# Performance work log

Hardware: AMD Instinct MI355X
Metric: run time of the kernel (lower is better)

Reference implementation:

```python
import jax, jax.numpy as jnp
import numpy as np

D_MODEL = 1024
NUM_HEADS = 16
D_K = D_MODEL // NUM_HEADS
ROPE_THETA = 10000.0


def setup_inputs() -> dict:
    key = jax.random.key(0)
    kx, kq, kk, kv, ko = jax.random.split(key, 5)
    B, S = 4, 2048
    std = (2.0 / (D_MODEL + D_MODEL)) ** 0.5
    def w(k):
        return jax.random.truncated_normal(k, -3.0, 3.0, (D_MODEL, D_MODEL), jnp.float32) * std
    return {
        "x": jax.random.normal(kx, (B, S, D_MODEL), jnp.float32),
        "Wq": w(kq), "Wk": w(kk), "Wv": w(kv), "Wo": w(ko),
    }


def _apply_rope(t):
    # t: [B, H, S, d_k]
    S, dk = t.shape[-2], t.shape[-1]
    inv_freq = 1.0 / (ROPE_THETA ** (jnp.arange(0, dk, 2) / dk))  # [dk/2]
    angles = jnp.outer(jnp.arange(S), inv_freq)                    # [S, dk/2]
    cos = jnp.repeat(jnp.cos(angles), 2, axis=-1).astype(t.dtype)  # [S, dk]
    sin = jnp.repeat(jnp.sin(angles), 2, axis=-1).astype(t.dtype)
    t_even = t[..., 0::2]
    t_odd = t[..., 1::2]
    t_rot = jnp.stack([-t_odd, t_even], axis=-1).reshape(t.shape)
    return t * cos + t_rot * sin


def reference(x, Wq, Wk, Wv, Wo):
    B, S, D = x.shape
    H, dk = NUM_HEADS, D_K
    q = jnp.einsum("bsi,io->bso", x, Wq).reshape(B, S, H, dk).swapaxes(1, 2)
    k = jnp.einsum("bsi,io->bso", x, Wk).reshape(B, S, H, dk).swapaxes(1, 2)
    v = jnp.einsum("bsi,io->bso", x, Wv).reshape(B, S, H, dk).swapaxes(1, 2)
    q = _apply_rope(q)
    k = _apply_rope(k)
    scores = jnp.einsum("bhqd,bhkd->bhqk", q, k) / (dk ** 0.5)  # [B,H,S,S]
    causal = jnp.tril(jnp.ones((S, S), dtype=bool))
    scores = jnp.where(causal, scores, -jnp.inf)
    attn = jax.nn.softmax(scores, axis=-1)
    out = jnp.einsum("bhqk,bhkd->bhqd", attn, v)  # [B,H,S,dk]
    out = out.swapaxes(1, 2).reshape(B, S, D)
    return jnp.einsum("bsi,io->bso", out, Wo)
```

## Files before the change

kernel.cpp:

```cpp
#include <hip/hip_runtime.h>
#include <hip/hip_bf16.h>

#define SEQ   2048
#define NB    4
#define NH    16
#define DK    64
#define DM    1024
#define MROWS (NB * SEQ)

typedef __bf16 bf16_t;
typedef __bf16 bf16x8 __attribute__((ext_vector_type(8)));
typedef __bf16 bf16x4 __attribute__((ext_vector_type(4)));
typedef float  f32x4  __attribute__((ext_vector_type(4)));

#define MFMA16(a, b, c) __builtin_amdgcn_mfma_f32_16x16x32_bf16((a), (b), (c), 0, 0, 0)

__device__ __forceinline__ void gl2lds16(const bf16_t* g, bf16_t* l) {
    __builtin_amdgcn_global_load_lds(
        (const __attribute__((address_space(1))) unsigned int*)g,
        (__attribute__((address_space(3))) unsigned int*)l, 16, 0, 0);
}

__global__ __launch_bounds__(256) void cvt_kernel(
    const float* __restrict__ in, bf16_t* __restrict__ out, int n)
{
    int i = (blockIdx.x * 256 + threadIdx.x) * 4;
    if (i + 3 < n) {
        const float4 v = *(const float4*)(in + i);
        bf16x4 o;
        o[0] = (bf16_t)v.x; o[1] = (bf16_t)v.y;
        o[2] = (bf16_t)v.z; o[3] = (bf16_t)v.w;
        *(bf16x4*)(out + i) = o;
    }
}

__global__ __launch_bounds__(256) void wtr_kernel(
    const float* __restrict__ W, bf16_t* __restrict__ Wt)
{
    __shared__ float T[32][33];
    const int tk0 = (blockIdx.x >> 5) << 5;
    const int tn0 = (blockIdx.x & 31) << 5;
    const int r = threadIdx.x >> 5, c = threadIdx.x & 31;
#pragma unroll
    for (int i = 0; i < 4; ++i)
        T[r + i * 8][c] = W[(size_t)(tk0 + r + i * 8) * DM + tn0 + c];
    __syncthreads();
#pragma unroll
    for (int i = 0; i < 4; ++i)
        Wt[(size_t)(tn0 + r + i * 8) * DM + tk0 + c] = (bf16_t)T[c][r + i * 8];
}

__global__ void rope_table_kernel(float2* __restrict__ tab) {
    int idx = blockIdx.x * 256 + threadIdx.x;
    if (idx >= SEQ * 32) return;
    int s = idx >> 5, i = idx & 31;
    float freq = powf(10000.0f, -(float)i / 32.0f);
    float a = (float)s * freq;
    tab[idx] = make_float2(cosf(a), sinf(a));
}

template<bool TR>
__device__ __forceinline__ void kloop128(
    const bf16_t* __restrict__ Xp, const bf16_t* __restrict__ Wp,
    bf16_t* As, bf16_t* Bs, int tid, f32x4 (&acc)[4][4], int kiters)
{
    const int lane = tid & 63;
    const int wave = tid >> 6;
    const int wm = wave & 1, wn = wave >> 1;
    const int l = lane & 15, quad = lane >> 4;
    const int rl = lane & 15;
    const int kf = (lane >> 4) << 3;
    const int gA = wave * 2;

    const bf16_t* xa0 = Xp + (size_t)(gA * 16 + rl) * DM + kf;
    const bf16_t* xa1 = Xp + (size_t)((gA + 1) * 16 + rl) * DM + kf;
    const bf16_t* wb0 = Wp + (size_t)(gA * 16 + rl) * DM + kf;
    const bf16_t* wb1 = Wp + (size_t)((gA + 1) * 16 + rl) * DM + kf;

    gl2lds16(xa0, As + gA * 512);
    gl2lds16(xa1, As + (gA + 1) * 512);
    gl2lds16(wb0, Bs + gA * 512);
    gl2lds16(wb1, Bs + (gA + 1) * 512);

    for (int k = 0; k < kiters; ++k) {
        const int cur = k & 1;
        __syncthreads();
        if (k + 1 < kiters) {
            const int nxt = cur ^ 1;
            const int ko = (k + 1) * 32;
            gl2lds16(xa0 + ko, As + nxt * 4096 + gA * 512);
            gl2lds16(xa1 + ko, As + nxt * 4096 + (gA + 1) * 512);
            gl2lds16(wb0 + ko, Bs + nxt * 4096 + gA * 512);
            gl2lds16(wb1 + ko, Bs + nxt * 4096 + (gA + 1) * 512);
        }
        const bf16_t* ab = As + cur * 4096;
        const bf16_t* bb = Bs + cur * 4096;
        bf16x8 af[4], bw[4];
#pragma unroll
        for (int a = 0; a < 4; ++a) {
            af[a] = *(const bf16x8*)(ab + (wm * 4 + a) * 512 + (quad * 16 + l) * 8);
            bw[a] = *(const bf16x8*)(bb + (wn * 4 + a) * 512 + (quad * 16 + l) * 8);
        }
#pragma unroll
        for (int a = 0; a < 4; ++a)
#pragma unroll
            for (int b = 0; b < 4; ++b)
                acc[a][b] = TR ? MFMA16(bw[b], af[a], acc[a][b])
                               : MFMA16(af[a], bw[b], acc[a][b]);
    }
}

__global__ __launch_bounds__(256) void gemm_qkv_kernel(
    const bf16_t* __restrict__ X, const bf16_t* __restrict__ Wt,
    bf16_t* __restrict__ Qt, bf16_t* __restrict__ Kt, bf16_t* __restrict__ Vtr,
    const float2* __restrict__ rope)
{
    __shared__ __align__(16) bf16_t As[2 * 128 * 32];
    __shared__ __align__(16) bf16_t Bs[2 * 128 * 32];

    const int tid  = threadIdx.x;
    const int lane = tid & 63;
    const int wave = tid >> 6;
    const int wm   = wave & 1, wn = wave >> 1;
    const int l    = lane & 15;
    const int quad = lane >> 4;

    const int m0 = (blockIdx.x / 24) << 7;
    const int n0 = (blockIdx.x % 24) << 7;
    const bool tr = (n0 >= 2 * DM);

    f32x4 acc[4][4] = {};
    if (tr) kloop128<true >(X + (size_t)m0 * DM, Wt + (size_t)n0 * DM, As, Bs, tid, acc, DM / 32);
    else    kloop128<false>(X + (size_t)m0 * DM, Wt + (size_t)n0 * DM, As, Bs, tid, acc, DM / 32);

#pragma unroll
    for (int a = 0; a < 4; ++a)
#pragma unroll
        for (int b = 0; b < 4; ++b)
#pragma unroll
            for (int r = 0; r < 4; ++r) {
                float v = acc[a][b][r];
                if (tr) {
                    const int n = n0 + wn * 64 + b * 16 + quad * 4 + r;
                    const int m = m0 + wm * 64 + a * 16 + l;
                    const int bi = m >> 11, s = m & (SEQ - 1);
                    const int col = n & (DM - 1);
                    const int h = col >> 6, d = col & (DK - 1);
                    Vtr[(((size_t)(bi * NH + h)) * DK + d) * SEQ + s] = (bf16_t)v;
                } else {
                    const int m  = m0 + wm * 64 + a * 16 + quad * 4 + r;
                    const int nn = n0 + wn * 64 + b * 16 + l;
                    const int bi = m >> 11, s = m & (SEQ - 1);
                    const int col = nn & (DM - 1);
                    const int h = col >> 6, d = col & (DK - 1);
                    float pv = __shfl_xor(v, 1);
                    float2 cs = rope[s * 32 + (d >> 1)];
                    float res = (d & 1) ? (v * cs.x + pv * cs.y)
                                        : (v * cs.x - pv * cs.y);
                    bf16_t* dst = (nn < DM) ? Qt : Kt;
                    if (nn < DM) res *= 0.125f;
                    dst[(((size_t)(bi * NH + h)) * SEQ + s) * DK + d] = (bf16_t)res;
                }
            }
}

__global__ __launch_bounds__(256) void gemm_out_kernel(
    const bf16_t* __restrict__ X, const bf16_t* __restrict__ Wt,
    float* __restrict__ out)
{
    __shared__ __align__(16) bf16_t As[2 * 128 * 32];
    __shared__ __align__(16) bf16_t Bs[2 * 128 * 32];

    const int tid  = threadIdx.x;
    const int lane = tid & 63;
    const int wave = tid >> 6;
    const int wm   = wave & 1, wn = wave >> 1;
    const int l    = lane & 15;
    const int quad = lane >> 4;

    const int m0 = (blockIdx.x >> 3) << 7;
    const int n0 = (blockIdx.x & 7) << 7;

    f32x4 acc[4][4] = {};
    kloop128<false>(X + (size_t)m0 * DM, Wt + (size_t)n0 * DM, As, Bs, tid, acc, DM / 32);

#pragma unroll
    for (int a = 0; a < 4; ++a)
#pragma unroll
        for (int b = 0; b < 4; ++b)
#pragma unroll
            for (int r = 0; r < 4; ++r) {
                const int m  = m0 + wm * 64 + a * 16 + quad * 4 + r;
                const int nn = n0 + wn * 64 + b * 16 + l;
                out[(size_t)m * DM + nn] = acc[a][b][r];
            }
}

#define KLD 72

__global__ __launch_bounds__(256) void attn_kernel(
    const bf16_t* __restrict__ Q, const bf16_t* __restrict__ K,
    const bf16_t* __restrict__ Vt, bf16_t* __restrict__ O)
{
    __shared__ __align__(16) bf16_t Kl[64 * KLD];
    __shared__ __align__(16) bf16_t Vl[64 * KLD];
    __shared__ __align__(16) bf16_t Pl[4][32 * KLD];

    const int bh   = blockIdx.y;
    const int tid  = threadIdx.x;
    const int wave = tid >> 6;
    const int lane = tid & 63;
    const int l    = lane & 15;
    const int quad = lane >> 4;
    const int srow = tid >> 3;
    const int sch  = (tid & 7) << 3;

    bf16_t* Pw = Pl[wave];
    const bf16_t* Qb = Q  + (size_t)bh * SEQ * DK;
    const bf16_t* Kb = K  + (size_t)bh * SEQ * DK;
    const bf16_t* Vb = Vt + (size_t)bh * DK * SEQ;
    const int b = bh >> 4, h = bh & 15;

    for (int ph = 0; ph < 2; ++ph) {
        const int qblk = ph ? (15 - (int)blockIdx.x) : (int)blockIdx.x;
        const int q0w  = qblk * 128 + wave * 32;
        const int nch  = 2 * (qblk + 1);

        bf16x8 qb[2][2];
#pragma unroll
        for (int u = 0; u < 2; ++u) {
            qb[u][0] = *(const bf16x8*)(Qb + (size_t)(q0w + u * 16 + l) * DK + quad * 8);
            qb[u][1] = *(const bf16x8*)(Qb + (size_t)(q0w + u * 16 + l) * DK + 32 + quad * 8);
        }

        float m_run[2] = {-3e38f, -3e38f};
        float l_run[2] = {0.f, 0.f};
        f32x4 o[4][2] = {};

        bf16x8 pk0 = *(const bf16x8*)(Kb + (size_t)srow * DK + sch);
        bf16x8 pk1 = *(const bf16x8*)(Kb + (size_t)(32 + srow) * DK + sch);
        bf16x8 pv0 = *(const bf16x8*)(Vb + (size_t)srow * SEQ + sch);
        bf16x8 pv1 = *(const bf16x8*)(Vb + (size_t)(32 + srow) * SEQ + sch);

        for (int i = 0; i < nch; ++i) {
            const int c = i * 64;
            __syncthreads();
            *(bf16x8*)(Kl + srow * KLD + sch)        = pk0;
            *(bf16x8*)(Kl + (32 + srow) * KLD + sch) = pk1;
            *(bf16x8*)(Vl + srow * KLD + sch)        = pv0;
            *(bf16x8*)(Vl + (32 + srow) * KLD + sch) = pv1;
            __syncthreads();
            if (i + 1 < nch) {
                const int cn = c + 64;
                pk0 = *(const bf16x8*)(Kb + (size_t)(cn + srow) * DK + sch);
                pk1 = *(const bf16x8*)(Kb + (size_t)(cn + 32 + srow) * DK + sch);
                pv0 = *(const bf16x8*)(Vb + (size_t)srow * SEQ + cn + sch);
                pv1 = *(const bf16x8*)(Vb + (size_t)(32 + srow) * SEQ + cn + sch);
            }
            if (c > q0w + 31) continue;

            f32x4 st[4][2] = {};
#pragma unroll
            for (int t = 0; t < 4; ++t) {
                const bf16x8 k0 = *(const bf16x8*)(Kl + (t * 16 + l) * KLD + quad * 8);
                const bf16x8 k1 = *(const bf16x8*)(Kl + (t * 16 + l) * KLD + 32 + quad * 8);
                st[t][0] = MFMA16(k0, qb[0][0], st[t][0]);
                st[t][0] = MFMA16(k1, qb[0][1], st[t][0]);
                st[t][1] = MFMA16(k0, qb[1][0], st[t][1]);
                st[t][1] = MFMA16(k1, qb[1][1], st[t][1]);
            }
            if (c + 63 > q0w) {
#pragma unroll
                for (int u = 0; u < 2; ++u) {
                    const int thr = q0w + u * 16 + l - c - quad * 4;
#pragma unroll
                    for (int t = 0; t < 4; ++t)
#pragma unroll
                        for (int r = 0; r < 4; ++r)
                            if (t * 16 + r > thr) st[t][u][r] = -3e38f;
                }
            }
#pragma unroll
            for (int u = 0; u < 2; ++u) {
                float cmax = -3e38f;
#pragma unroll
                for (int t = 0; t < 4; ++t)
#pragma unroll
                    for (int r = 0; r < 4; ++r)
                        cmax = fmaxf(cmax, st[t][u][r]);
                cmax = fmaxf(cmax, __shfl_xor(cmax, 16));
                cmax = fmaxf(cmax, __shfl_xor(cmax, 32));
                const float mnew  = fmaxf(m_run[u], cmax);
                const float alpha = __expf(m_run[u] - mnew);
                m_run[u] = mnew;
                float csum = 0.f;
#pragma unroll
                for (int t = 0; t < 4; ++t)
#pragma unroll
                    for (int r = 0; r < 4; ++r) {
                        st[t][u][r] = __expf(st[t][u][r] - mnew);
                        csum += st[t][u][r];
                    }
                csum += __shfl_xor(csum, 16);
                csum += __shfl_xor(csum, 32);
                l_run[u] = l_run[u] * alpha + csum;
#pragma unroll
                for (int n = 0; n < 4; ++n)
#pragma unroll
                    for (int r = 0; r < 4; ++r)
                        o[n][u][r] *= alpha;
#pragma unroll
                for (int t = 0; t < 4; ++t) {
                    bf16x4 pk;
                    pk[0] = (bf16_t)st[t][u][0]; pk[1] = (bf16_t)st[t][u][1];
                    pk[2] = (bf16_t)st[t][u][2]; pk[3] = (bf16_t)st[t][u][3];
                    *(bf16x4*)(Pw + (u * 16 + l) * KLD + t * 16 + quad * 4) = pk;
                }
            }
            const bf16x8 pb00 = *(const bf16x8*)(Pw + l * KLD + quad * 8);
            const bf16x8 pb01 = *(const bf16x8*)(Pw + l * KLD + 32 + quad * 8);
            const bf16x8 pb10 = *(const bf16x8*)(Pw + (16 + l) * KLD + quad * 8);
            const bf16x8 pb11 = *(const bf16x8*)(Pw + (16 + l) * KLD + 32 + quad * 8);
#pragma unroll
            for (int n = 0; n < 4; ++n) {
                const bf16x8 v0 = *(const bf16x8*)(Vl + (n * 16 + l) * KLD + quad * 8);
                const bf16x8 v1 = *(const bf16x8*)(Vl + (n * 16 + l) * KLD + 32 + quad * 8);
                o[n][0] = MFMA16(v0, pb00, o[n][0]);
                o[n][0] = MFMA16(v1, pb01, o[n][0]);
                o[n][1] = MFMA16(v0, pb10, o[n][1]);
                o[n][1] = MFMA16(v1, pb11, o[n][1]);
            }
        }

#pragma unroll
        for (int u = 0; u < 2; ++u) {
            const float inv = 1.0f / l_run[u];
#pragma unroll
            for (int n = 0; n < 4; ++n) {
                bf16x4 ov;
                ov[0] = (bf16_t)(o[n][u][0] * inv); ov[1] = (bf16_t)(o[n][u][1] * inv);
                ov[2] = (bf16_t)(o[n][u][2] * inv); ov[3] = (bf16_t)(o[n][u][3] * inv);
                *(bf16x4*)(Pw + (u * 16 + l) * KLD + n * 16 + quad * 4) = ov;
            }
        }
        const int row  = lane >> 1;
        const int half = (lane & 1) * 32;
        const bf16x8 w0 = *(const bf16x8*)(Pw + row * KLD + half);
        const bf16x8 w1 = *(const bf16x8*)(Pw + row * KLD + half + 8);
        const bf16x8 w2 = *(const bf16x8*)(Pw + row * KLD + half + 16);
        const bf16x8 w3 = *(const bf16x8*)(Pw + row * KLD + half + 24);
        bf16_t* op = O + ((size_t)(b * SEQ + qblk * 128 + wave * 32 + row)) * DM
                       + h * DK + half;
        *(bf16x8*)(op)      = w0;
        *(bf16x8*)(op + 8)  = w1;
        *(bf16x8*)(op + 16) = w2;
        *(bf16x8*)(op + 24) = w3;
    }
}

extern "C" void kernel_launch(void* const* d_in, const int* in_sizes, int n_in,
                              void* d_out, int out_size, void* d_ws, size_t ws_size,
                              hipStream_t stream)
{
    const float* x  = (const float*)d_in[0];
    const float* Wq = (const float*)d_in[1];
    const float* Wk = (const float*)d_in[2];
    const float* Wv = (const float*)d_in[3];
    const float* Wo = (const float*)d_in[4];

    char* ws = (char*)d_ws;
    float2* rope = (float2*)ws;
    const size_t TEN = (size_t)MROWS * DM;
    const size_t WEL = (size_t)DM * DM;
    bf16_t* xb    = (bf16_t*)(ws + (1 << 19));
    bf16_t* Wqkvt = xb + TEN;
    bf16_t* Wot   = Wqkvt + 3 * WEL;
    bf16_t* Qt    = Wot + WEL;
    bf16_t* Kt    = Qt + TEN;
    bf16_t* Vt    = Kt + TEN;
    bf16_t* Ot    = Vt + TEN;

    rope_table_kernel<<<(SEQ * 32 + 255) / 256, 256, 0, stream>>>(rope);

    cvt_kernel<<<(int)(TEN / 4 / 256), 256, 0, stream>>>(x, xb, (int)TEN);
    wtr_kernel<<<1024, 256, 0, stream>>>(Wq, Wqkvt);
    wtr_kernel<<<1024, 256, 0, stream>>>(Wk, Wqkvt + WEL);
    wtr_kernel<<<1024, 256, 0, stream>>>(Wv, Wqkvt + 2 * WEL);
    wtr_kernel<<<1024, 256, 0, stream>>>(Wo, Wot);

    gemm_qkv_kernel<<<64 * 24, 256, 0, stream>>>(xb, Wqkvt, Qt, Kt, Vt, rope);

    attn_kernel<<<dim3(8, NB * NH), 256, 0, stream>>>(Qt, Kt, Vt, Ot);

    gemm_out_kernel<<<64 * 8, 256, 0, stream>>>(Ot, Wot, (float*)d_out);
}
```

Baseline: 338.3 us.

## Shrink GEMM tiles to 128x64, reorder blocks M-fastest, merge weight transposes

Changes the QKV and output projection GEMMs from 128x128 to 128x64 output tiles. This doubles the grid size and, with launch_bounds of 4, is meant to raise occupancy, since the output GEMM previously launched only 512 blocks. Block indexing now iterates M fastest, so consecutive blocks share the same weight tile in L2. The four weight-transpose launches are merged into one 2D-grid kernel. The trade-off is lower arithmetic intensity per block and more total A-tile traffic.

```diff
diff --git a/kernel.cpp b/kernel.cpp
--- a/kernel.cpp
+++ b/kernel.cpp
@@ -34,10 +34,15 @@
     }
 }
 
-__global__ __launch_bounds__(256) void wtr_kernel(
-    const float* __restrict__ W, bf16_t* __restrict__ Wt)
+__global__ __launch_bounds__(256) void wtr4_kernel(
+    const float* __restrict__ W0, const float* __restrict__ W1,
+    const float* __restrict__ W2, const float* __restrict__ W3,
+    bf16_t* __restrict__ Wt)
 {
     __shared__ float T[32][33];
+    const int y = blockIdx.y;
+    const float* W = (y == 0) ? W0 : (y == 1) ? W1 : (y == 2) ? W2 : W3;
+    bf16_t* out = Wt + (size_t)y * DM * DM;
     const int tk0 = (blockIdx.x >> 5) << 5;
     const int tn0 = (blockIdx.x & 31) << 5;
     const int r = threadIdx.x >> 5, c = threadIdx.x & 31;
@@ -47,7 +52,7 @@
     __syncthreads();
 #pragma unroll
     for (int i = 0; i < 4; ++i)
-        Wt[(size_t)(tn0 + r + i * 8) * DM + tk0 + c] = (bf16_t)T[c][r + i * 8];
+        out[(size_t)(tn0 + r + i * 8) * DM + tk0 + c] = (bf16_t)T[c][r + i * 8];
 }
 
 __global__ void rope_table_kernel(float2* __restrict__ tab) {
@@ -60,9 +65,9 @@
 }
 
 template<bool TR>
-__device__ __forceinline__ void kloop128(
+__device__ __forceinline__ void kloop_128x64(
     const bf16_t* __restrict__ Xp, const bf16_t* __restrict__ Wp,
-    bf16_t* As, bf16_t* Bs, int tid, f32x4 (&acc)[4][4], int kiters)
+    bf16_t* As, bf16_t* Bs, int tid, f32x4 (&acc)[4][2])
 {
     const int lane = tid & 63;
     const int wave = tid >> 6;
@@ -70,53 +75,51 @@
     const int l = lane & 15, quad = lane >> 4;
     const int rl = lane & 15;
     const int kf = (lane >> 4) << 3;
-    const int gA = wave * 2;
-
-    const bf16_t* xa0 = Xp + (size_t)(gA * 16 + rl) * DM + kf;
-    const bf16_t* xa1 = Xp + (size_t)((gA + 1) * 16 + rl) * DM + kf;
-    const bf16_t* wb0 = Wp + (size_t)(gA * 16 + rl) * DM + kf;
-    const bf16_t* wb1 = Wp + (size_t)((gA + 1) * 16 + rl) * DM + kf;
-
-    gl2lds16(xa0, As + gA * 512);
-    gl2lds16(xa1, As + (gA + 1) * 512);
-    gl2lds16(wb0, Bs + gA * 512);
-    gl2lds16(wb1, Bs + (gA + 1) * 512);
-
+
+    const bf16_t* xa0 = Xp + (size_t)((wave * 2)     * 16 + rl) * DM + kf;
+    const bf16_t* xa1 = Xp + (size_t)((wave * 2 + 1) * 16 + rl) * DM + kf;
+    const bf16_t* wb0 = Wp + (size_t)(wave * 16 + rl) * DM + kf;
+
+    gl2lds16(xa0, As + (wave * 2) * 512);
+    gl2lds16(xa1, As + (wave * 2 + 1) * 512);
+    gl2lds16(wb0, Bs + wave * 512);
+
+    const int kiters = DM / 32;
     for (int k = 0; k < kiters; ++k) {
         const int cur = k & 1;
         __syncthreads();
         if (k + 1 < kiters) {
             const int nxt = cur ^ 1;
             const int ko = (k + 1) * 32;
-            gl2lds16(xa0 + ko, As + nxt * 4096 + gA * 512);
-            gl2lds16(xa1 + ko, As + nxt * 4096 + (gA + 1) * 512);
-            gl2lds16(wb0 + ko, Bs + nxt * 4096 + gA * 512);
-            gl2lds16(wb1 + ko, Bs + nxt * 4096 + (gA + 1) * 512);
+            gl2lds16(xa0 + ko, As + nxt * 4096 + (wave * 2) * 512);
+            gl2lds16(xa1 + ko, As + nxt * 4096 + (wave * 2 + 1) * 512);
+            gl2lds16(wb0 + ko, Bs + nxt * 2048 + wave * 512);
         }
         const bf16_t* ab = As + cur * 4096;
-        const bf16_t* bb = Bs + cur * 4096;
-        bf16x8 af[4], bw[4];
-#pragma unroll
-        for (int a = 0; a < 4; ++a) {
+        const bf16_t* bb = Bs + cur * 2048;
+        bf16x8 af[4], bw[2];
+#pragma unroll
+        for (int a = 0; a < 4; ++a)
             af[a] = *(const bf16x8*)(ab + (wm * 4 + a) * 512 + (quad * 16 + l) * 8);
-            bw[a] = *(const bf16x8*)(bb + (wn * 4 + a) * 512 + (quad * 16 + l) * 8);
-        }
+#pragma unroll
+        for (int b = 0; b < 2; ++b)
+            bw[b] = *(const bf16x8*)(bb + (wn * 2 + b) * 512 + (quad * 16 + l) * 8);
 #pragma unroll
         for (int a = 0; a < 4; ++a)
 #pragma unroll
-            for (int b = 0; b < 4; ++b)
+            for (int b = 0; b < 2; ++b)
                 acc[a][b] = TR ? MFMA16(bw[b], af[a], acc[a][b])
                                : MFMA16(af[a], bw[b], acc[a][b]);
     }
 }
 
-__global__ __launch_bounds__(256) void gemm_qkv_kernel(
+__global__ __launch_bounds__(256, 4) void gemm_qkv_kernel(
     const bf16_t* __restrict__ X, const bf16_t* __restrict__ Wt,
     bf16_t* __restrict__ Qt, bf16_t* __restrict__ Kt, bf16_t* __restrict__ Vtr,
     const float2* __restrict__ rope)
 {
     __shared__ __align__(16) bf16_t As[2 * 128 * 32];
-    __shared__ __align__(16) bf16_t Bs[2 * 128 * 32];
+    __shared__ __align__(16) bf16_t Bs[2 * 64 * 32];
 
     const int tid  = threadIdx.x;
     const int lane = tid & 63;
@@ -125,23 +128,23 @@
     const int l    = lane & 15;
     const int quad = lane >> 4;
 
-    const int m0 = (blockIdx.x / 24) << 7;
-    const int n0 = (blockIdx.x % 24) << 7;
+    const int n0 = (blockIdx.x >> 6) << 6;
+    const int m0 = (blockIdx.x & 63) << 7;
     const bool tr = (n0 >= 2 * DM);
 
-    f32x4 acc[4][4] = {};
-    if (tr) kloop128<true >(X + (size_t)m0 * DM, Wt + (size_t)n0 * DM, As, Bs, tid, acc, DM / 32);
-    else    kloop128<false>(X + (size_t)m0 * DM, Wt + (size_t)n0 * DM, As, Bs, tid, acc, DM / 32);
+    f32x4 acc[4][2] = {};
+    if (tr) kloop_128x64<true >(X + (size_t)m0 * DM, Wt + (size_t)n0 * DM, As, Bs, tid, acc);
+    else    kloop_128x64<false>(X + (size_t)m0 * DM, Wt + (size_t)n0 * DM, As, Bs, tid, acc);
 
 #pragma unroll
     for (int a = 0; a < 4; ++a)
 #pragma unroll
-        for (int b = 0; b < 4; ++b)
+        for (int b = 0; b < 2; ++b)
 #pragma unroll
             for (int r = 0; r < 4; ++r) {
                 float v = acc[a][b][r];
                 if (tr) {
-                    const int n = n0 + wn * 64 + b * 16 + quad * 4 + r;
+                    const int n = n0 + wn * 32 + b * 16 + quad * 4 + r;
                     const int m = m0 + wm * 64 + a * 16 + l;
                     const int bi = m >> 11, s = m & (SEQ - 1);
                     const int col = n & (DM - 1);
@@ -149,7 +152,7 @@
                     Vtr[(((size_t)(bi * NH + h)) * DK + d) * SEQ + s] = (bf16_t)v;
                 } else {
                     const int m  = m0 + wm * 64 + a * 16 + quad * 4 + r;
-                    const int nn = n0 + wn * 64 + b * 16 + l;
+                    const int nn = n0 + wn * 32 + b * 16 + l;
                     const int bi = m >> 11, s = m & (SEQ - 1);
                     const int col = nn & (DM - 1);
                     const int h = col >> 6, d = col & (DK - 1);
@@ -164,12 +167,12 @@
             }
 }
 
-__global__ __launch_bounds__(256) void gemm_out_kernel(
+__global__ __launch_bounds__(256, 4) void gemm_out_kernel(
     const bf16_t* __restrict__ X, const bf16_t* __restrict__ Wt,
     float* __restrict__ out)
 {
     __shared__ __align__(16) bf16_t As[2 * 128 * 32];
-    __shared__ __align__(16) bf16_t Bs[2 * 128 * 32];
+    __shared__ __align__(16) bf16_t Bs[2 * 64 * 32];
 
     const int tid  = threadIdx.x;
     const int lane = tid & 63;
@@ -178,20 +181,20 @@
     const int l    = lane & 15;
     const int quad = lane >> 4;
 
-    const int m0 = (blockIdx.x >> 3) << 7;
-    const int n0 = (blockIdx.x & 7) << 7;
-
-    f32x4 acc[4][4] = {};
-    kloop128<false>(X + (size_t)m0 * DM, Wt + (size_t)n0 * DM, As, Bs, tid, acc, DM / 32);
+    const int n0 = (blockIdx.x >> 6) << 6;
+    const int m0 = (blockIdx.x & 63) << 7;
+
+    f32x4 acc[4][2] = {};
+    kloop_128x64<false>(X + (size_t)m0 * DM, Wt + (size_t)n0 * DM, As, Bs, tid, acc);
 
 #pragma unroll
     for (int a = 0; a < 4; ++a)
 #pragma unroll
-        for (int b = 0; b < 4; ++b)
+        for (int b = 0; b < 2; ++b)
 #pragma unroll
             for (int r = 0; r < 4; ++r) {
                 const int m  = m0 + wm * 64 + a * 16 + quad * 4 + r;
-                const int nn = n0 + wn * 64 + b * 16 + l;
+                const int nn = n0 + wn * 32 + b * 16 + l;
                 out[(size_t)m * DM + nn] = acc[a][b][r];
             }
 }
@@ -383,14 +386,11 @@
     rope_table_kernel<<<(SEQ * 32 + 255) / 256, 256, 0, stream>>>(rope);
 
     cvt_kernel<<<(int)(TEN / 4 / 256), 256, 0, stream>>>(x, xb, (int)TEN);
-    wtr_kernel<<<1024, 256, 0, stream>>>(Wq, Wqkvt);
-    wtr_kernel<<<1024, 256, 0, stream>>>(Wk, Wqkvt + WEL);
-    wtr_kernel<<<1024, 256, 0, stream>>>(Wv, Wqkvt + 2 * WEL);
-    wtr_kernel<<<1024, 256, 0, stream>>>(Wo, Wot);
-
-    gemm_qkv_kernel<<<64 * 24, 256, 0, stream>>>(xb, Wqkvt, Qt, Kt, Vt, rope);
+    wtr4_kernel<<<dim3(1024, 4), 256, 0, stream>>>(Wq, Wk, Wv, Wo, Wqkvt);
+
+    gemm_qkv_kernel<<<48 * 64, 256, 0, stream>>>(xb, Wqkvt, Qt, Kt, Vt, rope);
 
     attn_kernel<<<dim3(8, NB * NH), 256, 0, stream>>>(Qt, Kt, Vt, Ot);
 
-    gemm_out_kernel<<<64 * 8, 256, 0, stream>>>(Ot, Wot, (float*)d_out);
-}
+    gemm_out_kernel<<<16 * 64, 256, 0, stream>>>(Ot, Wot, (float*)d_out);
+}
```

Result: slower. 362.9 us (+7.3%).
